# Performance work log

Hardware: AMD Instinct MI355X
Metric: run time of the kernel (lower is better)

Reference implementation:

```python
import jax, jax.numpy as jnp
import numpy as np
from jax import lax


def setup_inputs() -> dict:
    key = jax.random.key(0)
    B, C = 16384, 8192
    values_memory = jax.random.uniform(key, (B, C), dtype=jnp.float32)
    return {"values_memory": values_memory, "no_selectors": 8}


def reference(values_memory, no_selectors):
    # torch.sort(...)[0][:, -k:] == top-k values per row (order within the
    # slice doesn't matter since it's summed). Use O(n) selection instead
    # of a full sort.
    topk_vals, _ = lax.top_k(values_memory, no_selectors)  # [B, k]
    return jnp.sum(1.0 - jnp.sum(topk_vals, axis=1))
```

## Files before the change

### kernel.cpp

```cpp
#include <hip/hip_runtime.h>
#include <hip/hip_bf16.h>
#include <math.h>


#define C_COLS 8192
#define BLOCK 256
#define ROWS_PER_BLOCK 4
#define K 8

__device__ __forceinline__ void ce(float& a, float& b) {
    const float hi = fmaxf(a, b);
    const float lo = fminf(a, b);
    a = hi; b = lo;
}

__device__ __forceinline__ void bitonic_sort8_desc(float (&c)[K]) {
    ce(c[0], c[4]); ce(c[1], c[5]); ce(c[2], c[6]); ce(c[3], c[7]);
    ce(c[0], c[2]); ce(c[1], c[3]); ce(c[4], c[6]); ce(c[5], c[7]);
    ce(c[0], c[1]); ce(c[2], c[3]); ce(c[4], c[5]); ce(c[6], c[7]);
}

__device__ __forceinline__ void merge8(float (&t)[K], const float (&o)[K]) {
    float c[K];
#pragma unroll
    for (int i = 0; i < K; ++i) c[i] = fmaxf(t[i], o[K - 1 - i]);
    bitonic_sort8_desc(c);
#pragma unroll
    for (int i = 0; i < K; ++i) t[i] = c[i];
}

__device__ __forceinline__ void merge4into8(float (&t)[K],
                                            float b0, float b1, float b2, float b3) {
    float c[K];
    c[0] = t[0]; c[1] = t[1]; c[2] = t[2]; c[3] = t[3];
    c[4] = fmaxf(t[4], b3);
    c[5] = fmaxf(t[5], b2);
    c[6] = fmaxf(t[6], b1);
    c[7] = fmaxf(t[7], b0);
    bitonic_sort8_desc(c);
#pragma unroll
    for (int i = 0; i < K; ++i) t[i] = c[i];
}

__global__ __launch_bounds__(BLOCK) void hl_topk_rows(const float* __restrict__ vals,
                                                      float* __restrict__ row_out) {
    const int wave = threadIdx.x >> 6;
    const int lane = threadIdx.x & 63;
    const int row  = blockIdx.x * ROWS_PER_BLOCK + wave;

    const float4* rowp = reinterpret_cast<const float4*>(vals + (size_t)row * C_COLS);

    float t[K];
#pragma unroll
    for (int i = 0; i < K; ++i) t[i] = -INFINITY;

#pragma unroll 4
    for (int j = 0; j < (C_COLS / 4) / 64; ++j) {
        float4 v = rowp[j * 64 + lane];
        ce(v.x, v.y); ce(v.z, v.w); ce(v.x, v.z); ce(v.y, v.w); ce(v.y, v.z);
        merge4into8(t, v.x, v.y, v.z, v.w);
    }

#pragma unroll
    for (int m = 1; m < 64; m <<= 1) {
        float o[K];
#pragma unroll
        for (int i = 0; i < K; ++i) o[i] = __shfl_xor(t[i], m, 64);
        merge8(t, o);
    }

    if (lane == 0) {
        float s = 0.0f;
#pragma unroll
        for (int i = 0; i < K; ++i) s += t[i];
        row_out[row] = 1.0f - s;
    }
}

#define RBLOCK 1024

__global__ __launch_bounds__(RBLOCK) void hl_reduce(const float* __restrict__ in,
                                                    float* __restrict__ out, int n) {
    float s = 0.0f;
    for (int i = threadIdx.x; i < n; i += RBLOCK) s += in[i];
#pragma unroll
    for (int m = 32; m >= 1; m >>= 1) s += __shfl_xor(s, m, 64);
    __shared__ float sm[RBLOCK / 64];
    if ((threadIdx.x & 63) == 0) sm[threadIdx.x >> 6] = s;
    __syncthreads();
    if (threadIdx.x == 0) {
        float r = 0.0f;
#pragma unroll
        for (int i = 0; i < RBLOCK / 64; ++i) r += sm[i];
        out[0] = r;
    }
}

extern "C" void kernel_launch(void* const* d_in, const int* in_sizes, int n_in,
                              void* d_out, int out_size, void* d_ws, size_t ws_size,
                              hipStream_t stream) {
    const float* vals = (const float*)d_in[0];
    float* out = (float*)d_out;

    const int B = in_sizes[0] / C_COLS;
    float* row_ws = (float*)d_ws;

    hl_topk_rows<<<B / ROWS_PER_BLOCK, BLOCK, 0, stream>>>(vals, row_ws);
    hl_reduce<<<1, RBLOCK, 0, stream>>>(row_ws, out, B);
}
```

Measured before the change: 105.0 us.

## Use nontemporal vector loads, deeper unroll, and per-block partial sums

The row-streaming loop now uses nontemporal 16-byte loads and unrolls by 8 instead of 4, aiming to raise memory-level parallelism on a purely bandwidth-bound read of 512 MB. Each block sums its four row results in shared memory and writes one partial, so the final single-block reduction reads a quarter as many values, using vectorized loads. This adds a __syncthreads per block and assumes the block count is divisible by 4.

```diff
diff --git a/kernel.cpp b/kernel.cpp
--- a/kernel.cpp
+++ b/kernel.cpp
@@ -7,6 +7,8 @@
 #define BLOCK 256
 #define ROWS_PER_BLOCK 4
 #define K 8
+
+typedef float f32x4 __attribute__((ext_vector_type(4)));
 
 __device__ __forceinline__ void ce(float& a, float& b) {
     const float hi = fmaxf(a, b);
@@ -43,22 +45,23 @@
 }
 
 __global__ __launch_bounds__(BLOCK) void hl_topk_rows(const float* __restrict__ vals,
-                                                      float* __restrict__ row_out) {
+                                                      float* __restrict__ block_out) {
     const int wave = threadIdx.x >> 6;
     const int lane = threadIdx.x & 63;
     const int row  = blockIdx.x * ROWS_PER_BLOCK + wave;
 
-    const float4* rowp = reinterpret_cast<const float4*>(vals + (size_t)row * C_COLS);
+    const f32x4* rowp = reinterpret_cast<const f32x4*>(vals + (size_t)row * C_COLS);
 
     float t[K];
 #pragma unroll
     for (int i = 0; i < K; ++i) t[i] = -INFINITY;
 
-#pragma unroll 4
+#pragma unroll 8
     for (int j = 0; j < (C_COLS / 4) / 64; ++j) {
-        float4 v = rowp[j * 64 + lane];
-        ce(v.x, v.y); ce(v.z, v.w); ce(v.x, v.z); ce(v.y, v.w); ce(v.y, v.z);
-        merge4into8(t, v.x, v.y, v.z, v.w);
+        f32x4 v = __builtin_nontemporal_load(rowp + j * 64 + lane);
+        float x = v[0], y = v[1], z = v[2], w = v[3];
+        ce(x, y); ce(z, w); ce(x, z); ce(y, w); ce(y, z);
+        merge4into8(t, x, y, z, w);
     }
 
 #pragma unroll
@@ -69,20 +72,32 @@
         merge8(t, o);
     }
 
+    __shared__ float sm[ROWS_PER_BLOCK];
     if (lane == 0) {
         float s = 0.0f;
 #pragma unroll
         for (int i = 0; i < K; ++i) s += t[i];
-        row_out[row] = 1.0f - s;
+        sm[wave] = 1.0f - s;
+    }
+    __syncthreads();
+    if (threadIdx.x == 0) {
+        float r = 0.0f;
+#pragma unroll
+        for (int i = 0; i < ROWS_PER_BLOCK; ++i) r += sm[i];
+        block_out[blockIdx.x] = r;
     }
 }
 
 #define RBLOCK 1024
 
 __global__ __launch_bounds__(RBLOCK) void hl_reduce(const float* __restrict__ in,
-                                                    float* __restrict__ out, int n) {
+                                                    float* __restrict__ out, int n4) {
+    const f32x4* in4 = reinterpret_cast<const f32x4*>(in);
     float s = 0.0f;
-    for (int i = threadIdx.x; i < n; i += RBLOCK) s += in[i];
+    for (int i = threadIdx.x; i < n4; i += RBLOCK) {
+        f32x4 v = in4[i];
+        s += (v[0] + v[1]) + (v[2] + v[3]);
+    }
 #pragma unroll
     for (int m = 32; m >= 1; m >>= 1) s += __shfl_xor(s, m, 64);
     __shared__ float sm[RBLOCK / 64];
@@ -103,8 +118,9 @@
     float* out = (float*)d_out;
 
     const int B = in_sizes[0] / C_COLS;
-    float* row_ws = (float*)d_ws;
+    const int nblocks = B / ROWS_PER_BLOCK;
+    float* part_ws = (float*)d_ws;
 
-    hl_topk_rows<<<B / ROWS_PER_BLOCK, BLOCK, 0, stream>>>(vals, row_ws);
-    hl_reduce<<<1, RBLOCK, 0, stream>>>(row_ws, out, B);
+    hl_topk_rows<<<nblocks, BLOCK, 0, stream>>>(vals, part_ws);
+    hl_reduce<<<1, RBLOCK, 0, stream>>>(part_ws, out, nblocks / 4);
 }
```

Result: faster. 90.52 us (median of 2 runs) (-13.8%).
